# Performance work log

Hardware: AMD Instinct MI355X
Metric: run time of the kernel (lower is better)

Reference implementation:

```python
import math
import jax, jax.numpy as jnp
import numpy as np

B, D, C = 2, 1024, 512          # (b*f with f=1), spatial tokens, channels
H, DH = 8, 64                   # heads, head dim (H*DH == C)
P = 32                          # past length == temporal_max_len
MAX_LEN = 32
HID = max(128, C // 2)          # refiner hidden

def make_pe():
    # sinusoidal APE buffer, shape [MAX_LEN, C]
    position = np.arange(MAX_LEN)[:, None].astype(np.float32)
    div_term = np.exp(np.arange(0, C, 2).astype(np.float32) * (-math.log(10000.0) / C))
    pe = np.zeros((MAX_LEN, C), dtype=np.float32)
    pe[:, 0::2] = np.sin(position * div_term)
    pe[:, 1::2] = np.cos(position * div_term)
    return jnp.asarray(pe)

def setup_inputs() -> dict:
    key = jax.random.key(0)
    ks = jax.random.split(key, 12)
    sc = 0.02
    return {
        "hidden_states": jax.random.normal(ks[0], (B, D, C), jnp.float32),
        "cached_hidden_states": jax.random.normal(ks[1], (B * D, P, C), jnp.float32),
        "Wq": jax.random.normal(ks[2], (C, C), jnp.float32) * sc,
        "Wk": jax.random.normal(ks[3], (C, C), jnp.float32) * sc,
        "Wv": jax.random.normal(ks[4], (C, C), jnp.float32) * sc,
        "Wo": jax.random.normal(ks[5], (C, C), jnp.float32) * sc,
        "bo": jnp.zeros((C,), jnp.float32),
        "W1": jax.random.normal(ks[6], (3 * C, HID), jnp.float32) * sc,
        "b1": jnp.zeros((HID,), jnp.float32),
        "W2": jax.random.normal(ks[7], (HID, 2 * C + 2), jnp.float32) * sc,
        "b2": jnp.zeros((2 * C + 2,), jnp.float32),
        "pe": make_pe(),
        "select_top_r": 8,
    }

def reference(hidden_states, cached_hidden_states, Wq, Wk, Wv, Wo, bo, W1, b1, W2, b2, pe, select_top_r):
    b, d, c = hidden_states.shape
    B0 = b * d
    # '(b f) d c -> (b d) f c' with f=1
    now = hidden_states.reshape(B0, 1, c)
    past = cached_hidden_states                      # [B0, P, C]
    # APE positional encoding
    now_pos = now + pe[:1][None]
    past_pos = past + pe[: past.shape[1]][None]
    # projections (no bias, diffusers CrossAttention style)
    q_now = now_pos @ Wq                             # [B0, 1, C]
    k_now = now_pos @ Wk
    v_now = now_pos @ Wv
    k_past = past_pos @ Wk                           # [B0, P, C]
    v_past = past_pos @ Wv
    # top-r key selection over past
    score = jnp.einsum('bqc,bpc->bqp', q_now, k_past)[:, 0]   # [B0, P]
    _, idx = jax.lax.top_k(score, select_top_r)               # [B0, R]
    k_sel = jnp.take_along_axis(k_past, idx[:, :, None], axis=1)  # [B0, R, C]
    v_sel = jnp.take_along_axis(v_past, idx[:, :, None], axis=1)
    # refiner MLP: concat(q, k, v) -> hidden -> 2C+2
    R = k_sel.shape[1]
    q_rep = jnp.broadcast_to(q_now, (B0, R, c))
    inp = jnp.concatenate([q_rep, k_sel, v_sel], axis=-1)     # [B0, R, 3C]
    h = jax.nn.gelu(inp @ W1 + b1, approximate=False)
    out = h @ W2 + b2                                         # [B0, R, 2C+2]
    dK, dV, log_s, logit_g = jnp.split(out, [c, 2 * c, 2 * c + 1], axis=-1)
    s = jax.nn.softplus(log_s) + 1e-5
    g = jax.nn.sigmoid(logit_g)
    k_sel = k_sel + g * dK * s
    v_sel = v_sel + g * dV * s
    # attention over [selected past ; now]
    key_ = jnp.concatenate([k_sel, k_now], axis=1)            # [B0, R+1, C]
    val_ = jnp.concatenate([v_sel, v_now], axis=1)
    L = key_.shape[1]
    qh = q_now.reshape(B0, 1, H, DH)
    kh = key_.reshape(B0, L, H, DH)
    vh = val_.reshape(B0, L, H, DH)
    scale = DH ** -0.5
    logits = jnp.einsum('bqhd,bkhd->bhqk', qh, kh) * scale
    attn = jax.nn.softmax(logits, axis=-1)
    ctx = jnp.einsum('bhqk,bkhd->bqhd', attn, vh).reshape(B0, 1, c)
    out_proj = ctx @ Wo + bo                                  # [B0, 1, C]
    # '(b d) f c -> (b f) d c' with f=1
    return out_proj.reshape(b, d, c)
```

## Files before the change

### kernel.cpp

```cpp
#include <hip/hip_runtime.h>
#include <math.h>


typedef __attribute__((ext_vector_type(8))) __bf16 bf16x8;
typedef __attribute__((ext_vector_type(4))) float f32x4;
typedef unsigned short u16;
typedef unsigned int u32;

static __device__ __forceinline__ float4 ld4(const float* p) { return *(const float4*)p; }
static __device__ __forceinline__ float gelu_exact(float x) {
  return 0.5f * x * (1.0f + erff(x * 0.70710678118654752f));
}
static __device__ __forceinline__ u16 f2bf(float f) {
  u32 u = __float_as_uint(f);
  u = (u + 0x7fffu + ((u >> 16) & 1u)) >> 16;
  return (u16)u;
}
static __device__ __forceinline__ float bf2f(u16 h) {
  return __uint_as_float(((u32)h) << 16);
}
static __device__ __forceinline__ u32 pk2(float a, float b) {
  return (u32)f2bf(a) | ((u32)f2bf(b) << 16);
}
static __device__ __forceinline__ void ld8bf(const u16* p, float* o) {
  int4 v = *(const int4*)p;
  o[0] = bf2f((u16)((u32)v.x & 0xffffu)); o[1] = bf2f((u16)(((u32)v.x) >> 16));
  o[2] = bf2f((u16)((u32)v.y & 0xffffu)); o[3] = bf2f((u16)(((u32)v.y) >> 16));
  o[4] = bf2f((u16)((u32)v.z & 0xffffu)); o[5] = bf2f((u16)(((u32)v.z) >> 16));
  o[6] = bf2f((u16)((u32)v.w & 0xffffu)); o[7] = bf2f((u16)(((u32)v.w) >> 16));
}
static __device__ __forceinline__ void gld16(const void* g, void* l) {
  __builtin_amdgcn_global_load_lds((const __attribute__((address_space(1))) void*)g,
                                   (__attribute__((address_space(3))) void*)l, 16, 0, 0);
}
template <int NI>
static __device__ __forceinline__ void stageT(u16* __restrict__ lds,
                                              const u16* __restrict__ sp,
                                              int ldk, int w) {
#pragma unroll
  for (int i = 0; i < NI; ++i)
    gld16(sp + (size_t)(i << 5) * ldk, lds + (w << 9) + (i << 11));
}

__global__ __launch_bounds__(256) void prep_all(
    const float* __restrict__ Wq, const float* __restrict__ Wk,
    const float* __restrict__ Wv, const float* __restrict__ W1,
    const float* __restrict__ W2, const float* __restrict__ Wo,
    u16* __restrict__ Wqkvt, u16* __restrict__ W1t,
    u16* __restrict__ W2t, u16* __restrict__ Wot,
    float* __restrict__ Wqk) {
  const int b = blockIdx.x;
  if (b < 1664) {
    __shared__ float t[32][33];
    const float* S; u16* D; int lds_, Kd, nx, t0;
    if (b < 256)       { S = Wq; D = Wqkvt;              lds_ = 512;  Kd = 512;  nx = 16; t0 = 0; }
    else if (b < 512)  { S = Wk; D = Wqkvt + 512 * 512;  lds_ = 512;  Kd = 512;  nx = 16; t0 = 256; }
    else if (b < 768)  { S = Wv; D = Wqkvt + 1024 * 512; lds_ = 512;  Kd = 512;  nx = 16; t0 = 512; }
    else if (b < 1152) { S = W1; D = W1t;                lds_ = 256;  Kd = 1536; nx = 8;  t0 = 768; }
    else if (b < 1408) { S = W2; D = W2t;                lds_ = 1026; Kd = 256;  nx = 32; t0 = 1152; }
    else               { S = Wo; D = Wot;                lds_ = 512;  Kd = 512;  nx = 16; t0 = 1408; }
    const int tile = b - t0;
    const int n0 = (tile % nx) << 5, k0 = (tile / nx) << 5;
    const int tx = threadIdx.x & 31, ty8 = threadIdx.x >> 5;
    for (int yy = ty8; yy < 32; yy += 8)
      t[yy][tx] = S[(size_t)(k0 + yy) * lds_ + n0 + tx];
    __syncthreads();
    for (int yy = ty8; yy < 32; yy += 8)
      D[(size_t)(n0 + yy) * Kd + k0 + tx] = f2bf(t[tx][yy]);
  } else {
    __shared__ float Aq[32][36];
    __shared__ float Bk[32][36];
    const int tile = b - 1664;
    const int c0 = (tile >> 4) << 5, j0 = (tile & 15) << 5;
    const int tid = threadIdx.x;
    const int r = tid >> 3, ic = (tid & 7) << 2;
    const int ty = tid >> 4, tx = tid & 15;
    float a00 = 0.f, a01 = 0.f, a10 = 0.f, a11 = 0.f;
    for (int i0 = 0; i0 < 512; i0 += 32) {
      float4 a = ld4(Wq + (size_t)(c0 + r) * 512 + i0 + ic);
      float4 bb = ld4(Wk + (size_t)(j0 + r) * 512 + i0 + ic);
      Aq[r][ic] = a.x; Aq[r][ic + 1] = a.y; Aq[r][ic + 2] = a.z; Aq[r][ic + 3] = a.w;
      Bk[r][ic] = bb.x; Bk[r][ic + 1] = bb.y; Bk[r][ic + 2] = bb.z; Bk[r][ic + 3] = bb.w;
      __syncthreads();
#pragma unroll
      for (int i = 0; i < 32; ++i) {
        float x0 = Aq[ty * 2][i], x1 = Aq[ty * 2 + 1][i];
        float y0 = Bk[tx * 2][i], y1 = Bk[tx * 2 + 1][i];
        a00 += x0 * y0; a01 += x0 * y1; a10 += x1 * y0; a11 += x1 * y1;
      }
      __syncthreads();
    }
    Wqk[(size_t)(c0 + ty * 2) * 512 + j0 + tx * 2]         = a00;
    Wqk[(size_t)(c0 + ty * 2) * 512 + j0 + tx * 2 + 1]     = a01;
    Wqk[(size_t)(c0 + ty * 2 + 1) * 512 + j0 + tx * 2]     = a10;
    Wqk[(size_t)(c0 + ty * 2 + 1) * 512 + j0 + tx * 2 + 1] = a11;
  }
}

__global__ __launch_bounds__(256) void qk_gemm(const float* __restrict__ A,
                                               const float* __restrict__ B,
                                               float* __restrict__ C,
                                               const float* __restrict__ pe) {
  __shared__ float As[16][68];
  __shared__ float Bs[16][68];
  const int tid = threadIdx.x;
  const int rm = blockIdx.y << 6, cn = blockIdx.x << 6;
  const int tx = tid & 15, ty = tid >> 4;
  const int ar = tid >> 2, ak = (tid & 3) << 2;
  const int bk = tid >> 4, bn = (tid & 15) << 2;
  const float* Ap = A + (size_t)(rm + ar) * 512;
  float acc[4][4] = {};
  for (int kt = 0; kt < 32; ++kt) {
    const int k0 = (kt << 4) + ak;
    float4 x = ld4(Ap + k0);
    float4 p4 = ld4(pe + k0);
    As[ak + 0][ar] = x.x + p4.x; As[ak + 1][ar] = x.y + p4.y;
    As[ak + 2][ar] = x.z + p4.z; As[ak + 3][ar] = x.w + p4.w;
    *(float4*)&Bs[bk][bn] = ld4(B + (size_t)((kt << 4) + bk) * 512 + cn + bn);
    __syncthreads();
#pragma unroll
    for (int kk = 0; kk < 16; ++kk) {
      float4 a = *(const float4*)&As[kk][ty << 2];
      float4 b = *(const float4*)&Bs[kk][tx << 2];
      acc[0][0] += a.x * b.x; acc[0][1] += a.x * b.y; acc[0][2] += a.x * b.z; acc[0][3] += a.x * b.w;
      acc[1][0] += a.y * b.x; acc[1][1] += a.y * b.y; acc[1][2] += a.y * b.z; acc[1][3] += a.y * b.w;
      acc[2][0] += a.z * b.x; acc[2][1] += a.z * b.y; acc[2][2] += a.z * b.z; acc[2][3] += a.z * b.w;
      acc[3][0] += a.w * b.x; acc[3][1] += a.w * b.y; acc[3][2] += a.w * b.z; acc[3][3] += a.w * b.w;
    }
    __syncthreads();
  }
  const int row0 = rm + (ty << 2), col0 = cn + (tx << 2);
#pragma unroll
  for (int i = 0; i < 4; ++i)
    *(float4*)(C + (size_t)(row0 + i) * 512 + col0) =
        make_float4(acc[i][0], acc[i][1], acc[i][2], acc[i][3]);
}

__global__ __launch_bounds__(256) void score_topk_gather(
    const float* __restrict__ QK, const float* __restrict__ cached,
    const float* __restrict__ pe, const float* __restrict__ hidden,
    u16* __restrict__ xh, u16* __restrict__ gsel) {
  __shared__ float sc[32];
  __shared__ int ix[8];
  const int b0 = blockIdx.x;
  const int tid = threadIdx.x;
  const int w = tid >> 6, lane = tid & 63;
  const int off = lane << 3;
  const float* qk = QK + (size_t)b0 * 512;
  float4 q0 = ld4(qk + off);
  float4 q1 = ld4(qk + off + 4);
  for (int i = 0; i < 8; ++i) {
    const int p = (w << 3) + i;
    const float* cp = cached + ((size_t)b0 * 32 + p) * 512 + off;
    const float* pp = pe + (size_t)p * 512 + off;
    float4 c0 = ld4(cp), c1 = ld4(cp + 4);
    float4 e0 = ld4(pp), e1 = ld4(pp + 4);
    float s = (c0.x + e0.x) * q0.x + (c0.y + e0.y) * q0.y +
              (c0.z + e0.z) * q0.z + (c0.w + e0.w) * q0.w +
              (c1.x + e1.x) * q1.x + (c1.y + e1.y) * q1.y +
              (c1.z + e1.z) * q1.z + (c1.w + e1.w) * q1.w;
#pragma unroll
    for (int d = 32; d > 0; d >>= 1) s += __shfl_xor(s, d);
    if (lane == 0) sc[p] = s;
  }
  __syncthreads();
  if (tid == 0) {
    for (int r = 0; r < 8; ++r) {
      float best = -INFINITY; int bi = 0;
      for (int p = 0; p < 32; ++p) {
        float v = sc[p];
        if (v > best) { best = v; bi = p; }
      }
      ix[r] = bi;
      sc[bi] = -INFINITY;
    }
  }
  __syncthreads();
#pragma unroll
  for (int rr = 0; rr < 2; ++rr) {
    const int rsel = w + (rr << 2);
    const int p = ix[rsel];
    const float* cp = cached + ((size_t)b0 * 32 + p) * 512 + off;
    const float* pp = pe + (size_t)p * 512 + off;
    float4 c0 = ld4(cp), c1 = ld4(cp + 4);
    float4 e0 = ld4(pp), e1 = ld4(pp + 4);
    int4 o;
    o.x = pk2(c0.x + e0.x, c0.y + e0.y);
    o.y = pk2(c0.z + e0.z, c0.w + e0.w);
    o.z = pk2(c1.x + e1.x, c1.y + e1.y);
    o.w = pk2(c1.z + e1.z, c1.w + e1.w);
    *(int4*)(gsel + (size_t)(b0 * 8 + rsel) * 512 + off) = o;
  }
  if (w == 0) {
    const float* hp = hidden + (size_t)b0 * 512 + off;
    float4 a = ld4(hp), b = ld4(hp + 4);
    float4 p0 = ld4(pe + off), p1 = ld4(pe + off + 4);
    int4 o;
    o.x = pk2(a.x + p0.x, a.y + p0.y);
    o.y = pk2(a.z + p0.z, a.w + p0.w);
    o.z = pk2(b.x + p1.x, b.y + p1.y);
    o.w = pk2(b.z + p1.z, b.w + p1.w);
    *(int4*)(xh + (size_t)b0 * 512 + off) = o;
  }
}

__global__ __launch_bounds__(256) void bgemm_fused1(
    const u16* __restrict__ gsel, const u16* __restrict__ xh,
    const u16* __restrict__ Wqkvt, u16* __restrict__ kvh,
    u16* __restrict__ Yh) {
  __shared__ u16 As[8192];
  __shared__ u16 Bs[8192];
  const int tid = threadIdx.x, lane = tid & 63, w = tid >> 6;
  const int bid = blockIdx.x;
  int rm, cn, ldc; const u16 *Ab, *Bb; u16* C;
  if (bid < 1024) {
    rm = (bid >> 3) << 7; cn = (bid & 7) << 7;
    Ab = gsel; Bb = Wqkvt + (size_t)512 * 512; C = kvh; ldc = 1024;
  } else {
    const int b2 = bid - 1024;
    rm = (b2 / 12) << 7; cn = (b2 % 12) << 7;
    Ab = xh; Bb = Wqkvt; C = Yh; ldc = 1536;
  }
  const int lrow = (w << 3) + (lane >> 3), lko = (lane & 7) << 3;
  const u16* ap = Ab + (size_t)(rm + lrow) * 512 + lko;
  const u16* bp = Bb + (size_t)(cn + lrow) * 512 + lko;
  const int aoff = ((w >> 1) << 12) + ((lane & 15) << 6) + ((lane >> 4) << 3);
  const int boff = ((w & 1) << 12) + ((lane & 15) << 6) + ((lane >> 4) << 3);
  f32x4 acc[4][4];
#pragma unroll
  for (int i = 0; i < 4; ++i)
#pragma unroll
    for (int j = 0; j < 4; ++j) acc[i][j] = (f32x4){0.f, 0.f, 0.f, 0.f};
  for (int kt = 0; kt < 8; ++kt) {
    if (kt) __syncthreads();
    stageT<4>(As, ap, 512, w);
    stageT<4>(Bs, bp, 512, w);
    ap += 64; bp += 64;
    __syncthreads();
#pragma unroll
    for (int s = 0; s < 2; ++s) {
      bf16x8 av[4], bv[4];
#pragma unroll
      for (int i = 0; i < 4; ++i) av[i] = *(const bf16x8*)(As + aoff + (i << 10) + (s << 5));
#pragma unroll
      for (int j = 0; j < 4; ++j) bv[j] = *(const bf16x8*)(Bs + boff + (j << 10) + (s << 5));
#pragma unroll
      for (int i = 0; i < 4; ++i)
#pragma unroll
        for (int j = 0; j < 4; ++j)
          acc[i][j] = __builtin_amdgcn_mfma_f32_16x16x32_bf16(bv[j], av[i], acc[i][j], 0, 0, 0);
    }
  }
  const int row0 = rm + ((w >> 1) << 6) + (lane & 15);
  const int col0 = cn + ((w & 1) << 6) + ((lane >> 4) << 2);
#pragma unroll
  for (int i = 0; i < 4; ++i) {
    u16* cp = C + (size_t)(row0 + (i << 4)) * ldc + col0;
#pragma unroll
    for (int j = 0; j < 4; ++j) {
      int2 o;
      o.x = (int)pk2(acc[i][j][0], acc[i][j][1]);
      o.y = (int)pk2(acc[i][j][2], acc[i][j][3]);
      *(int2*)(cp + (j << 4)) = o;
    }
  }
}

__global__ __launch_bounds__(256) void mlp1_sg(
    const u16* __restrict__ Yh, const u16* __restrict__ kvh,
    const u16* __restrict__ W1t, const float* __restrict__ b1,
    const float* __restrict__ W2, const float* __restrict__ b2,
    u16* __restrict__ hb, float* __restrict__ sgv) {
  __shared__ u16 As[4096];
  __shared__ u16 Bs[16384];
  __shared__ float wa[256], wb[256];
  const int tid = threadIdx.x, lane = tid & 63, w = tid >> 6;
  const int rm = blockIdx.x << 6;
  wa[tid] = W2[(size_t)tid * 1026 + 1024];
  wb[tid] = W2[(size_t)tid * 1026 + 1025];
  const int lrow = (w << 3) + (lane >> 3), lko = (lane & 7) << 3;
  const u16* aq0  = Yh + (size_t)((rm + lrow) >> 3) * 1536 + lko;
  const u16* aq1  = Yh + (size_t)((rm + lrow + 32) >> 3) * 1536 + lko;
  const u16* akv0 = kvh + (size_t)(rm + lrow) * 1024 + lko;
  const u16* akv1 = kvh + (size_t)(rm + lrow + 32) * 1024 + lko;
  const u16* bp = W1t + (size_t)lrow * 1536 + lko;
  const int aoff = ((lane & 15) << 6) + ((lane >> 4) << 3);
  const int boff = (w << 12) + aoff;
  f32x4 acc[4][4];
#pragma unroll
  for (int i = 0; i < 4; ++i)
#pragma unroll
    for (int j = 0; j < 4; ++j) acc[i][j] = (f32x4){0.f, 0.f, 0.f, 0.f};
  for (int kt = 0; kt < 24; ++kt) {
    const int ko = kt << 6;
    if (kt) __syncthreads();
    if (kt < 8) {
      gld16(aq0 + ko, As + (w << 9));
      gld16(aq1 + ko, As + (w << 9) + 2048);
    } else {
      gld16(akv0 + ko - 512, As + (w << 9));
      gld16(akv1 + ko - 512, As + (w << 9) + 2048);
    }
    stageT<8>(Bs, bp, 1536, w);
    bp += 64;
    __syncthreads();
#pragma unroll
    for (int s = 0; s < 2; ++s) {
      bf16x8 av[4], bv[4];
#pragma unroll
      for (int i = 0; i < 4; ++i) av[i] = *(const bf16x8*)(As + aoff + (i << 10) + (s << 5));
#pragma unroll
      for (int j = 0; j < 4; ++j) bv[j] = *(const bf16x8*)(Bs + boff + (j << 10) + (s << 5));
#pragma unroll
      for (int i = 0; i < 4; ++i)
#pragma unroll
        for (int j = 0; j < 4; ++j)
          acc[i][j] = __builtin_amdgcn_mfma_f32_16x16x32_bf16(bv[j], av[i], acc[i][j], 0, 0, 0);
    }
  }
  const int row0 = rm + (lane & 15);
  const int col0 = (w << 6) + ((lane >> 4) << 2);
#pragma unroll
  for (int i = 0; i < 4; ++i) {
    u16* hp = hb + (size_t)(row0 + (i << 4)) * 256 + col0;
#pragma unroll
    for (int j = 0; j < 4; ++j) {
      float4 bb = ld4(b1 + col0 + (j << 4));
      int2 o;
      o.x = (int)pk2(gelu_exact(acc[i][j][0] + bb.x), gelu_exact(acc[i][j][1] + bb.y));
      o.y = (int)pk2(gelu_exact(acc[i][j][2] + bb.z), gelu_exact(acc[i][j][3] + bb.w));
      *(int2*)(hp + (j << 4)) = o;
    }
  }
  __syncthreads();
  const int row = tid >> 2, q = tid & 3;
  const int rr = rm + row;
  const u16* hp = hb + (size_t)rr * 256 + (q << 6);
  float pa = 0.f, pb = 0.f;
  for (int c = 0; c < 64; c += 8) {
    float h[8]; ld8bf(hp + c, h);
    const int cb = (q << 6) + c;
#pragma unroll
    for (int t = 0; t < 8; ++t) { pa += h[t] * wa[cb + t]; pb += h[t] * wb[cb + t]; }
  }
  pa += __shfl_xor(pa, 1); pa += __shfl_xor(pa, 2);
  pb += __shfl_xor(pb, 1); pb += __shfl_xor(pb, 2);
  if (q == 0) {
    const float t0 = pa + b2[1024];
    const float t1 = pb + b2[1025];
    const float s = (t0 > 0.f ? t0 + log1pf(expf(-t0)) : log1pf(expf(t0))) + 1e-5f;
    const float g = 1.f / (1.f + expf(-t1));
    sgv[2 * rr] = s; sgv[2 * rr + 1] = g;
  }
}

__global__ __launch_bounds__(256) void bgemm_delta(
    const u16* __restrict__ hb, const u16* __restrict__ W2t,
    u16* __restrict__ kvh, const float* __restrict__ b2,
    const float* __restrict__ sgv) {
  __shared__ u16 As[8192];
  __shared__ u16 Bs[8192];
  const int tid = threadIdx.x, lane = tid & 63, w = tid >> 6;
  const int rm = blockIdx.y << 7, cn = blockIdx.x << 7;
  const int lrow = (w << 3) + (lane >> 3), lko = (lane & 7) << 3;
  const u16* ap = hb + (size_t)(rm + lrow) * 256 + lko;
  const u16* bp = W2t + (size_t)(cn + lrow) * 256 + lko;
  const int aoff = ((w >> 1) << 12) + ((lane & 15) << 6) + ((lane >> 4) << 3);
  const int boff = ((w & 1) << 12) + ((lane & 15) << 6) + ((lane >> 4) << 3);
  f32x4 acc[4][4];
#pragma unroll
  for (int i = 0; i < 4; ++i)
#pragma unroll
    for (int j = 0; j < 4; ++j) acc[i][j] = (f32x4){0.f, 0.f, 0.f, 0.f};
  for (int kt = 0; kt < 4; ++kt) {
    if (kt) __syncthreads();
    stageT<4>(As, ap, 256, w);
    stageT<4>(Bs, bp, 256, w);
    ap += 64; bp += 64;
    __syncthreads();
#pragma unroll
    for (int s = 0; s < 2; ++s) {
      bf16x8 av[4], bv[4];
#pragma unroll
      for (int i = 0; i < 4; ++i) av[i] = *(const bf16x8*)(As + aoff + (i << 10) + (s << 5));
#pragma unroll
      for (int j = 0; j < 4; ++j) bv[j] = *(const bf16x8*)(Bs + boff + (j << 10) + (s << 5));
#pragma unroll
      for (int i = 0; i < 4; ++i)
#pragma unroll
        for (int j = 0; j < 4; ++j)
          acc[i][j] = __builtin_amdgcn_mfma_f32_16x16x32_bf16(bv[j], av[i], acc[i][j], 0, 0, 0);
    }
  }
  const int row0 = rm + ((w >> 1) << 6) + (lane & 15);
  const int col0 = cn + ((w & 1) << 6) + ((lane >> 4) << 2);
#pragma unroll
  for (int i = 0; i < 4; ++i) {
    const int row = row0 + (i << 4);
    const float2 sg2 = *(const float2*)(sgv + (row << 1));
    const float gs = sg2.x * sg2.y;
    u16* cp = kvh + (size_t)row * 1024 + col0;
#pragma unroll
    for (int j = 0; j < 4; ++j) {
      float4 bb = ld4(b2 + col0 + (j << 4));
      int2 old = *(const int2*)(cp + (j << 4));
      const float o0 = bf2f((u16)((u32)old.x & 0xffffu)) + gs * (acc[i][j][0] + bb.x);
      const float o1 = bf2f((u16)(((u32)old.x) >> 16)) + gs * (acc[i][j][1] + bb.y);
      const float o2 = bf2f((u16)((u32)old.y & 0xffffu)) + gs * (acc[i][j][2] + bb.z);
      const float o3 = bf2f((u16)(((u32)old.y) >> 16)) + gs * (acc[i][j][3] + bb.w);
      int2 nv;
      nv.x = (int)pk2(o0, o1);
      nv.y = (int)pk2(o2, o3);
      *(int2*)(cp + (j << 4)) = nv;
    }
  }
}

__global__ __launch_bounds__(256) void attn2(const u16* __restrict__ Yh,
                                             const u16* __restrict__ kvh,
                                             u16* __restrict__ ctxh) {
  const int w = threadIdx.x >> 6, lane = threadIdx.x & 63;
  const int b0 = (blockIdx.x << 2) + w;
  const int off = lane << 3;
  const u16* yr = Yh + (size_t)b0 * 1536;
  float qv[8]; ld8bf(yr + off, qv);
  float lg[9];
#pragma unroll
  for (int k = 0; k < 9; ++k) {
    const u16* kr = (k < 8) ? (kvh + (size_t)(b0 * 8 + k) * 1024 + off)
                            : (yr + 512 + off);
    float kv[8]; ld8bf(kr, kv);
    float s = qv[0] * kv[0] + qv[1] * kv[1] + qv[2] * kv[2] + qv[3] * kv[3] +
              qv[4] * kv[4] + qv[5] * kv[5] + qv[6] * kv[6] + qv[7] * kv[7];
    s += __shfl_xor(s, 1); s += __shfl_xor(s, 2); s += __shfl_xor(s, 4);
    lg[k] = s * 0.125f;
  }
  float m = lg[0];
#pragma unroll
  for (int k = 1; k < 9; ++k) m = fmaxf(m, lg[k]);
  float sum = 0.f;
#pragma unroll
  for (int k = 0; k < 9; ++k) { lg[k] = expf(lg[k] - m); sum += lg[k]; }
  const float inv = 1.f / sum;
  float c[8] = {0.f, 0.f, 0.f, 0.f, 0.f, 0.f, 0.f, 0.f};
#pragma unroll
  for (int k = 0; k < 9; ++k) {
    const u16* vr = (k < 8) ? (kvh + (size_t)(b0 * 8 + k) * 1024 + 512 + off)
                            : (yr + 1024 + off);
    float vv[8]; ld8bf(vr, vv);
    const float wk = lg[k] * inv;
#pragma unroll
    for (int t = 0; t < 8; ++t) c[t] += wk * vv[t];
  }
  int4 o;
  o.x = pk2(c[0], c[1]); o.y = pk2(c[2], c[3]);
  o.z = pk2(c[4], c[5]); o.w = pk2(c[6], c[7]);
  *(int4*)(ctxh + (size_t)b0 * 512 + off) = o;
}

__global__ __launch_bounds__(256) void bgemm_out(
    const u16* __restrict__ ctxh, const u16* __restrict__ Wot,
    float* __restrict__ out, const float* __restrict__ bo) {
  __shared__ u16 As[8192];
  __shared__ u16 Bs[8192];
  const int tid = threadIdx.x, lane = tid & 63, w = tid >> 6;
  const int rm = blockIdx.y << 7, cn = blockIdx.x << 7;
  const int lrow = (w << 3) + (lane >> 3), lko = (lane & 7) << 3;
  const u16* ap = ctxh + (size_t)(rm + lrow) * 512 + lko;
  const u16* bp = Wot + (size_t)(cn + lrow) * 512 + lko;
  const int aoff = ((w >> 1) << 12) + ((lane & 15) << 6) + ((lane >> 4) << 3);
  const int boff = ((w & 1) << 12) + ((lane & 15) << 6) + ((lane >> 4) << 3);
  f32x4 acc[4][4];
#pragma unroll
  for (int i = 0; i < 4; ++i)
#pragma unroll
    for (int j = 0; j < 4; ++j) acc[i][j] = (f32x4){0.f, 0.f, 0.f, 0.f};
  for (int kt = 0; kt < 8; ++kt) {
    if (kt) __syncthreads();
    stageT<4>(As, ap, 512, w);
    stageT<4>(Bs, bp, 512, w);
    ap += 64; bp += 64;
    __syncthreads();
#pragma unroll
    for (int s = 0; s < 2; ++s) {
      bf16x8 av[4], bv[4];
#pragma unroll
      for (int i = 0; i < 4; ++i) av[i] = *(const bf16x8*)(As + aoff + (i << 10) + (s << 5));
#pragma unroll
      for (int j = 0; j < 4; ++j) bv[j] = *(const bf16x8*)(Bs + boff + (j << 10) + (s << 5));
#pragma unroll
      for (int i = 0; i < 4; ++i)
#pragma unroll
        for (int j = 0; j < 4; ++j)
          acc[i][j] = __builtin_amdgcn_mfma_f32_16x16x32_bf16(bv[j], av[i], acc[i][j], 0, 0, 0);
    }
  }
  const int row0 = rm + ((w >> 1) << 6) + (lane & 15);
  const int col0 = cn + ((w & 1) << 6) + ((lane >> 4) << 2);
#pragma unroll
  for (int i = 0; i < 4; ++i) {
    float* op = out + (size_t)(row0 + (i << 4)) * 512 + col0;
#pragma unroll
    for (int j = 0; j < 4; ++j) {
      float4 bb = ld4(bo + col0 + (j << 4));
      *(float4*)(op + (j << 4)) = make_float4(acc[i][j][0] + bb.x, acc[i][j][1] + bb.y,
                                              acc[i][j][2] + bb.z, acc[i][j][3] + bb.w);
    }
  }
}

extern "C" void kernel_launch(void* const* d_in, const int* in_sizes, int n_in,
                              void* d_out, int out_size, void* d_ws, size_t ws_size,
                              hipStream_t stream) {
  const float* hidden = (const float*)d_in[0];
  const float* cached = (const float*)d_in[1];
  const float* Wq = (const float*)d_in[2];
  const float* Wk = (const float*)d_in[3];
  const float* Wv = (const float*)d_in[4];
  const float* Wo = (const float*)d_in[5];
  const float* bo = (const float*)d_in[6];
  const float* W1 = (const float*)d_in[7];
  const float* b1 = (const float*)d_in[8];
  const float* W2 = (const float*)d_in[9];
  const float* b2 = (const float*)d_in[10];
  const float* pe = (const float*)d_in[11];

  float* ws = (float*)d_ws;
  float* Wqk = ws;
  float* qkb = Wqk + 262144;
  float* sgv = qkb + 1048576;
  u16* Wqkvt = (u16*)(sgv + 32768);
  u16* W1t   = Wqkvt + 786432;
  u16* W2t   = W1t + 393216;
  u16* Wot   = W2t + 262144;
  u16* xh    = Wot + 262144;
  u16* gsel  = xh + 1048576;
  u16* Yh    = gsel + 8388608;
  u16* kvh   = Yh + 3145728;
  u16* hb    = kvh + 16777216;
  u16* ctxh  = hb + 4194304;
  float* out = (float*)d_out;
  (void)in_sizes; (void)n_in; (void)out_size; (void)ws_size;

  prep_all<<<dim3(1920), 256, 0, stream>>>(Wq, Wk, Wv, W1, W2, Wo,
                                           Wqkvt, W1t, W2t, Wot, Wqk);
  qk_gemm<<<dim3(8, 32), 256, 0, stream>>>(hidden, Wqk, qkb, pe);
  score_topk_gather<<<dim3(2048), 256, 0, stream>>>(qkb, cached, pe, hidden, xh, gsel);
  bgemm_fused1<<<dim3(1216), 256, 0, stream>>>(gsel, xh, Wqkvt, kvh, Yh);
  mlp1_sg<<<dim3(256), 256, 0, stream>>>(Yh, kvh, W1t, b1, W2, b2, hb, sgv);
  bgemm_delta<<<dim3(8, 128), 256, 0, stream>>>(hb, W2t, kvh, b2, sgv);
  attn2<<<dim3(512), 256, 0, stream>>>(Yh, kvh, ctxh);
  bgemm_out<<<dim3(4, 16), 256, 0, stream>>>(ctxh, Wot, out, bo);
}
```

Before: 452.9 us.

## XOR-swizzle LDS tiles in GEMMs, split mlp1 columns, move softplus/sigmoid into delta GEMM

Each bf16 MFMA GEMM now fetches its K chunks from global memory in an XOR-permuted order and reads LDS fragments with the matching XOR index. The aim is to remove LDS bank conflicts on the fragment loads. mlp1 is split across two 128-column blocks to double the grid size and halve its B tile. The per-row softplus/sigmoid scale-gate is moved from mlp1 into the delta GEMM prologue, which drops the sgv workspace round trip. In exchange, each column block now recomputes those row dot products redundantly and the delta kernel gains an extra barrier.

```diff
diff --git a/kernel.cpp b/kernel.cpp
--- a/kernel.cpp
+++ b/kernel.cpp
@@ -221,11 +221,12 @@
     rm = (b2 / 12) << 7; cn = (b2 % 12) << 7;
     Ab = xh; Bb = Wqkvt; C = Yh; ldc = 1536;
   }
-  const int lrow = (w << 3) + (lane >> 3), lko = (lane & 7) << 3;
-  const u16* ap = Ab + (size_t)(rm + lrow) * 512 + lko;
-  const u16* bp = Bb + (size_t)(cn + lrow) * 512 + lko;
-  const int aoff = ((w >> 1) << 12) + ((lane & 15) << 6) + ((lane >> 4) << 3);
-  const int boff = ((w & 1) << 12) + ((lane & 15) << 6) + ((lane >> 4) << 3);
+  const int lrow = (w << 3) + (lane >> 3);
+  const int skq8 = (((lane & 7) ^ ((lane >> 3) & 7)) << 3);
+  const u16* ap = Ab + (size_t)(rm + lrow) * 512 + skq8;
+  const u16* bp = Bb + (size_t)(cn + lrow) * 512 + skq8;
+  const int abase = ((w >> 1) << 12) + ((lane & 15) << 6);
+  const int bbase = ((w & 1) << 12) + ((lane & 15) << 6);
   f32x4 acc[4][4];
 #pragma unroll
   for (int i = 0; i < 4; ++i)
@@ -239,11 +240,12 @@
     __syncthreads();
 #pragma unroll
     for (int s = 0; s < 2; ++s) {
+      const int sq = ((((lane >> 4) | (s << 2)) ^ (lane & 7)) << 3);
       bf16x8 av[4], bv[4];
 #pragma unroll
-      for (int i = 0; i < 4; ++i) av[i] = *(const bf16x8*)(As + aoff + (i << 10) + (s << 5));
-#pragma unroll
-      for (int j = 0; j < 4; ++j) bv[j] = *(const bf16x8*)(Bs + boff + (j << 10) + (s << 5));
+      for (int i = 0; i < 4; ++i) av[i] = *(const bf16x8*)(As + abase + (i << 10) + sq);
+#pragma unroll
+      for (int j = 0; j < 4; ++j) bv[j] = *(const bf16x8*)(Bs + bbase + (j << 10) + sq);
 #pragma unroll
       for (int i = 0; i < 4; ++i)
 #pragma unroll
@@ -266,65 +268,63 @@
   }
 }
 
-__global__ __launch_bounds__(256) void mlp1_sg(
+__global__ __launch_bounds__(256) void mlp1(
     const u16* __restrict__ Yh, const u16* __restrict__ kvh,
     const u16* __restrict__ W1t, const float* __restrict__ b1,
-    const float* __restrict__ W2, const float* __restrict__ b2,
-    u16* __restrict__ hb, float* __restrict__ sgv) {
+    u16* __restrict__ hb) {
   __shared__ u16 As[4096];
-  __shared__ u16 Bs[16384];
-  __shared__ float wa[256], wb[256];
+  __shared__ u16 Bs[8192];
   const int tid = threadIdx.x, lane = tid & 63, w = tid >> 6;
-  const int rm = blockIdx.x << 6;
-  wa[tid] = W2[(size_t)tid * 1026 + 1024];
-  wb[tid] = W2[(size_t)tid * 1026 + 1025];
-  const int lrow = (w << 3) + (lane >> 3), lko = (lane & 7) << 3;
-  const u16* aq0  = Yh + (size_t)((rm + lrow) >> 3) * 1536 + lko;
-  const u16* aq1  = Yh + (size_t)((rm + lrow + 32) >> 3) * 1536 + lko;
-  const u16* akv0 = kvh + (size_t)(rm + lrow) * 1024 + lko;
-  const u16* akv1 = kvh + (size_t)(rm + lrow + 32) * 1024 + lko;
-  const u16* bp = W1t + (size_t)lrow * 1536 + lko;
-  const int aoff = ((lane & 15) << 6) + ((lane >> 4) << 3);
-  const int boff = (w << 12) + aoff;
-  f32x4 acc[4][4];
+  const int rm = blockIdx.y << 6, cn = blockIdx.x << 7;
+  const int lrow = (w << 3) + (lane >> 3);
+  const int skq8 = (((lane & 7) ^ ((lane >> 3) & 7)) << 3);
+  const u16* aq0  = Yh + (size_t)((rm + lrow) >> 3) * 1536 + skq8;
+  const u16* aq1  = Yh + (size_t)((rm + lrow + 32) >> 3) * 1536 + skq8;
+  const u16* akv0 = kvh + (size_t)(rm + lrow) * 1024 + skq8;
+  const u16* akv1 = kvh + (size_t)(rm + lrow + 32) * 1024 + skq8;
+  const u16* bp = W1t + (size_t)(cn + lrow) * 1536 + skq8;
+  const int abase = ((lane & 15) << 6);
+  const int bbase = (((w << 5) + (lane & 15)) << 6);
+  f32x4 acc[4][2];
 #pragma unroll
   for (int i = 0; i < 4; ++i)
 #pragma unroll
-    for (int j = 0; j < 4; ++j) acc[i][j] = (f32x4){0.f, 0.f, 0.f, 0.f};
+    for (int j = 0; j < 2; ++j) acc[i][j] = (f32x4){0.f, 0.f, 0.f, 0.f};
   for (int kt = 0; kt < 24; ++kt) {
     const int ko = kt << 6;
     if (kt) __syncthreads();
     if (kt < 8) {
       gld16(aq0 + ko, As + (w << 9));
-      gld16(aq1 + ko, As + (w << 9) + 2048);
+      gld16(aq1 + ko, As + 2048 + (w << 9));
     } else {
       gld16(akv0 + ko - 512, As + (w << 9));
-      gld16(akv1 + ko - 512, As + (w << 9) + 2048);
-    }
-    stageT<8>(Bs, bp, 1536, w);
+      gld16(akv1 + ko - 512, As + 2048 + (w << 9));
+    }
+    stageT<4>(Bs, bp, 1536, w);
     bp += 64;
     __syncthreads();
 #pragma unroll
     for (int s = 0; s < 2; ++s) {
-      bf16x8 av[4], bv[4];
-#pragma unroll
-      for (int i = 0; i < 4; ++i) av[i] = *(const bf16x8*)(As + aoff + (i << 10) + (s << 5));
-#pragma unroll
-      for (int j = 0; j < 4; ++j) bv[j] = *(const bf16x8*)(Bs + boff + (j << 10) + (s << 5));
+      const int sq = ((((lane >> 4) | (s << 2)) ^ (lane & 7)) << 3);
+      bf16x8 av[4], bv[2];
+#pragma unroll
+      for (int i = 0; i < 4; ++i) av[i] = *(const bf16x8*)(As + abase + (i << 10) + sq);
+#pragma unroll
+      for (int j = 0; j < 2; ++j) bv[j] = *(const bf16x8*)(Bs + bbase + (j << 10) + sq);
 #pragma unroll
       for (int i = 0; i < 4; ++i)
 #pragma unroll
-        for (int j = 0; j < 4; ++j)
+        for (int j = 0; j < 2; ++j)
           acc[i][j] = __builtin_amdgcn_mfma_f32_16x16x32_bf16(bv[j], av[i], acc[i][j], 0, 0, 0);
     }
   }
   const int row0 = rm + (lane & 15);
-  const int col0 = (w << 6) + ((lane >> 4) << 2);
+  const int col0 = cn + (w << 5) + ((lane >> 4) << 2);
 #pragma unroll
   for (int i = 0; i < 4; ++i) {
     u16* hp = hb + (size_t)(row0 + (i << 4)) * 256 + col0;
 #pragma unroll
-    for (int j = 0; j < 4; ++j) {
+    for (int j = 0; j < 2; ++j) {
       float4 bb = ld4(b1 + col0 + (j << 4));
       int2 o;
       o.x = (int)pk2(gelu_exact(acc[i][j][0] + bb.x), gelu_exact(acc[i][j][1] + bb.y));
@@ -332,46 +332,51 @@
       *(int2*)(hp + (j << 4)) = o;
     }
   }
-  __syncthreads();
-  const int row = tid >> 2, q = tid & 3;
-  const int rr = rm + row;
-  const u16* hp = hb + (size_t)rr * 256 + (q << 6);
-  float pa = 0.f, pb = 0.f;
-  for (int c = 0; c < 64; c += 8) {
-    float h[8]; ld8bf(hp + c, h);
-    const int cb = (q << 6) + c;
-#pragma unroll
-    for (int t = 0; t < 8; ++t) { pa += h[t] * wa[cb + t]; pb += h[t] * wb[cb + t]; }
-  }
-  pa += __shfl_xor(pa, 1); pa += __shfl_xor(pa, 2);
-  pb += __shfl_xor(pb, 1); pb += __shfl_xor(pb, 2);
-  if (q == 0) {
-    const float t0 = pa + b2[1024];
-    const float t1 = pb + b2[1025];
-    const float s = (t0 > 0.f ? t0 + log1pf(expf(-t0)) : log1pf(expf(t0))) + 1e-5f;
-    const float g = 1.f / (1.f + expf(-t1));
-    sgv[2 * rr] = s; sgv[2 * rr + 1] = g;
-  }
-}
-
-__global__ __launch_bounds__(256) void bgemm_delta(
+}
+
+__global__ __launch_bounds__(256) void bgemm_delta_sg(
     const u16* __restrict__ hb, const u16* __restrict__ W2t,
-    u16* __restrict__ kvh, const float* __restrict__ b2,
-    const float* __restrict__ sgv) {
+    u16* __restrict__ kvh, const float* __restrict__ W2,
+    const float* __restrict__ b2) {
   __shared__ u16 As[8192];
   __shared__ u16 Bs[8192];
+  __shared__ float wa_s[256], wb_s[256];
+  __shared__ float2 sg_s[128];
   const int tid = threadIdx.x, lane = tid & 63, w = tid >> 6;
   const int rm = blockIdx.y << 7, cn = blockIdx.x << 7;
-  const int lrow = (w << 3) + (lane >> 3), lko = (lane & 7) << 3;
-  const u16* ap = hb + (size_t)(rm + lrow) * 256 + lko;
-  const u16* bp = W2t + (size_t)(cn + lrow) * 256 + lko;
-  const int aoff = ((w >> 1) << 12) + ((lane & 15) << 6) + ((lane >> 4) << 3);
-  const int boff = ((w & 1) << 12) + ((lane & 15) << 6) + ((lane >> 4) << 3);
+  wa_s[tid] = W2[(size_t)tid * 1026 + 1024];
+  wb_s[tid] = W2[(size_t)tid * 1026 + 1025];
+  __syncthreads();
+  {
+    const int row = tid >> 1, sel = tid & 1;
+    const float* wsel = sel ? wb_s : wa_s;
+    const u16* hp = hb + (size_t)(rm + row) * 256;
+    float d = 0.f;
+    for (int c = 0; c < 256; c += 8) {
+      float h[8]; ld8bf(hp + c, h);
+#pragma unroll
+      for (int t = 0; t < 8; ++t) d += h[t] * wsel[c + t];
+    }
+    if (sel == 0) {
+      const float t0 = d + b2[1024];
+      sg_s[row].x = (t0 > 0.f ? t0 + log1pf(expf(-t0)) : log1pf(expf(t0))) + 1e-5f;
+    } else {
+      const float t1 = d + b2[1025];
+      sg_s[row].y = 1.f / (1.f + expf(-t1));
+    }
+  }
+  const int lrow = (w << 3) + (lane >> 3);
+  const int skq8 = (((lane & 7) ^ ((lane >> 3) & 7)) << 3);
+  const u16* ap = hb + (size_t)(rm + lrow) * 256 + skq8;
+  const u16* bp = W2t + (size_t)(cn + lrow) * 256 + skq8;
+  const int abase = ((w >> 1) << 12) + ((lane & 15) << 6);
+  const int bbase = ((w & 1) << 12) + ((lane & 15) << 6);
   f32x4 acc[4][4];
 #pragma unroll
   for (int i = 0; i < 4; ++i)
 #pragma unroll
     for (int j = 0; j < 4; ++j) acc[i][j] = (f32x4){0.f, 0.f, 0.f, 0.f};
+  __syncthreads();
   for (int kt = 0; kt < 4; ++kt) {
     if (kt) __syncthreads();
     stageT<4>(As, ap, 256, w);
@@ -380,11 +385,12 @@
     __syncthreads();
 #pragma unroll
     for (int s = 0; s < 2; ++s) {
+      const int sq = ((((lane >> 4) | (s << 2)) ^ (lane & 7)) << 3);
       bf16x8 av[4], bv[4];
 #pragma unroll
-      for (int i = 0; i < 4; ++i) av[i] = *(const bf16x8*)(As + aoff + (i << 10) + (s << 5));
-#pragma unroll
-      for (int j = 0; j < 4; ++j) bv[j] = *(const bf16x8*)(Bs + boff + (j << 10) + (s << 5));
+      for (int i = 0; i < 4; ++i) av[i] = *(const bf16x8*)(As + abase + (i << 10) + sq);
+#pragma unroll
+      for (int j = 0; j < 4; ++j) bv[j] = *(const bf16x8*)(Bs + bbase + (j << 10) + sq);
 #pragma unroll
       for (int i = 0; i < 4; ++i)
 #pragma unroll
@@ -392,14 +398,14 @@
           acc[i][j] = __builtin_amdgcn_mfma_f32_16x16x32_bf16(bv[j], av[i], acc[i][j], 0, 0, 0);
     }
   }
-  const int row0 = rm + ((w >> 1) << 6) + (lane & 15);
+  const int rloc0 = ((w >> 1) << 6) + (lane & 15);
   const int col0 = cn + ((w & 1) << 6) + ((lane >> 4) << 2);
 #pragma unroll
   for (int i = 0; i < 4; ++i) {
-    const int row = row0 + (i << 4);
-    const float2 sg2 = *(const float2*)(sgv + (row << 1));
+    const int rloc = rloc0 + (i << 4);
+    const float2 sg2 = sg_s[rloc];
     const float gs = sg2.x * sg2.y;
-    u16* cp = kvh + (size_t)row * 1024 + col0;
+    u16* cp = kvh + (size_t)(rm + rloc) * 1024 + col0;
 #pragma unroll
     for (int j = 0; j < 4; ++j) {
       float4 bb = ld4(b2 + col0 + (j << 4));
@@ -465,11 +471,12 @@
   __shared__ u16 Bs[8192];
   const int tid = threadIdx.x, lane = tid & 63, w = tid >> 6;
   const int rm = blockIdx.y << 7, cn = blockIdx.x << 7;
-  const int lrow = (w << 3) + (lane >> 3), lko = (lane & 7) << 3;
-  const u16* ap = ctxh + (size_t)(rm + lrow) * 512 + lko;
-  const u16* bp = Wot + (size_t)(cn + lrow) * 512 + lko;
-  const int aoff = ((w >> 1) << 12) + ((lane & 15) << 6) + ((lane >> 4) << 3);
-  const int boff = ((w & 1) << 12) + ((lane & 15) << 6) + ((lane >> 4) << 3);
+  const int lrow = (w << 3) + (lane >> 3);
+  const int skq8 = (((lane & 7) ^ ((lane >> 3) & 7)) << 3);
+  const u16* ap = ctxh + (size_t)(rm + lrow) * 512 + skq8;
+  const u16* bp = Wot + (size_t)(cn + lrow) * 512 + skq8;
+  const int abase = ((w >> 1) << 12) + ((lane & 15) << 6);
+  const int bbase = ((w & 1) << 12) + ((lane & 15) << 6);
   f32x4 acc[4][4];
 #pragma unroll
   for (int i = 0; i < 4; ++i)
@@ -483,11 +490,12 @@
     __syncthreads();
 #pragma unroll
     for (int s = 0; s < 2; ++s) {
+      const int sq = ((((lane >> 4) | (s << 2)) ^ (lane & 7)) << 3);
       bf16x8 av[4], bv[4];
 #pragma unroll
-      for (int i = 0; i < 4; ++i) av[i] = *(const bf16x8*)(As + aoff + (i << 10) + (s << 5));
-#pragma unroll
-      for (int j = 0; j < 4; ++j) bv[j] = *(const bf16x8*)(Bs + boff + (j << 10) + (s << 5));
+      for (int i = 0; i < 4; ++i) av[i] = *(const bf16x8*)(As + abase + (i << 10) + sq);
+#pragma unroll
+      for (int j = 0; j < 4; ++j) bv[j] = *(const bf16x8*)(Bs + bbase + (j << 10) + sq);
 #pragma unroll
       for (int i = 0; i < 4; ++i)
 #pragma unroll
@@ -528,8 +536,7 @@
   float* ws = (float*)d_ws;
   float* Wqk = ws;
   float* qkb = Wqk + 262144;
-  float* sgv = qkb + 1048576;
-  u16* Wqkvt = (u16*)(sgv + 32768);
+  u16* Wqkvt = (u16*)(qkb + 1048576);
   u16* W1t   = Wqkvt + 786432;
   u16* W2t   = W1t + 393216;
   u16* Wot   = W2t + 262144;
@@ -547,8 +554,8 @@
   qk_gemm<<<dim3(8, 32), 256, 0, stream>>>(hidden, Wqk, qkb, pe);
   score_topk_gather<<<dim3(2048), 256, 0, stream>>>(qkb, cached, pe, hidden, xh, gsel);
   bgemm_fused1<<<dim3(1216), 256, 0, stream>>>(gsel, xh, Wqkvt, kvh, Yh);
-  mlp1_sg<<<dim3(256), 256, 0, stream>>>(Yh, kvh, W1t, b1, W2, b2, hb, sgv);
-  bgemm_delta<<<dim3(8, 128), 256, 0, stream>>>(hb, W2t, kvh, b2, sgv);
+  mlp1<<<dim3(2, 256), 256, 0, stream>>>(Yh, kvh, W1t, b1, hb);
+  bgemm_delta_sg<<<dim3(8, 128), 256, 0, stream>>>(hb, W2t, kvh, W2, b2);
   attn2<<<dim3(512), 256, 0, stream>>>(Yh, kvh, ctxh);
   bgemm_out<<<dim3(4, 16), 256, 0, stream>>>(ctxh, Wot, out, bo);
 }
```

Result: faster. 441.4 us (-2.5%).
